# Kernel optimization log

Hardware: AMD Instinct MI355X
Metric: run time of the kernel (lower is better)

## Reference

```python
import jax, jax.numpy as jnp
import numpy as np

N_NODES = 10000
N_EDGES = 80000
F_IN = 128
H1 = 2048
H2 = 2048
H3 = 1024


def _sgconv(x, pos, src, dst, W_in, b_in, W_out, b_out):
    # geo-GCN SpatialGraphConv with hidden_size=1:
    # message(j->i) = relu(Linear(pos_j - pos_i)) * x_j ; aggr='add' ; then Linear out
    rel = pos[src] - pos[dst]                      # [E, 2]  (pos_j - pos_i)
    scale = jax.nn.relu(rel @ W_in + b_in)         # [E, C_in]
    msg = scale * x[src]                           # [E, C_in]
    agg = jax.ops.segment_sum(msg, dst, num_segments=x.shape[0])  # [N, C_in]
    return agg @ W_out + b_out                     # [N, C_out]


def setup_inputs() -> dict:
    key = jax.random.key(0)
    ks = jax.random.split(key, 12)
    x = jax.random.normal(ks[0], (N_NODES, F_IN), dtype=jnp.float32)
    pos = jax.random.normal(ks[1], (N_NODES, 2), dtype=jnp.float32)
    edge_index = jax.random.randint(ks[2], (2, N_EDGES), 0, N_NODES, dtype=jnp.int32)

    def lin(k, fan_in, fan_out):
        lim = 1.0 / np.sqrt(fan_in)
        kw, kb = jax.random.split(k)
        W = jax.random.uniform(kw, (fan_in, fan_out), jnp.float32, -lim, lim)
        b = jax.random.uniform(kb, (fan_out,), jnp.float32, -lim, lim)
        return W, b

    W_in1, b_in1 = lin(ks[3], 2, F_IN)
    W_out1, b_out1 = lin(ks[4], F_IN, H1)
    W_in2, b_in2 = lin(ks[5], 2, H1)
    W_out2, b_out2 = lin(ks[6], H1, H2)
    W_in3, b_in3 = lin(ks[7], 2, H2)
    W_out3, b_out3 = lin(ks[8], H2, H3)

    return {
        "x": x, "pos": pos, "edge_index": edge_index,
        "W_in1": W_in1, "b_in1": b_in1, "W_out1": W_out1, "b_out1": b_out1,
        "W_in2": W_in2, "b_in2": b_in2, "W_out2": W_out2, "b_out2": b_out2,
        "W_in3": W_in3, "b_in3": b_in3, "W_out3": W_out3, "b_out3": b_out3,
    }


def reference(x, pos, edge_index,
              W_in1, b_in1, W_out1, b_out1,
              W_in2, b_in2, W_out2, b_out2,
              W_in3, b_in3, W_out3, b_out3):
    src, dst = edge_index[0], edge_index[1]  # flow source_to_target: j=src, i=dst
    h = jax.nn.relu(_sgconv(x, pos, src, dst, W_in1, b_in1, W_out1, b_out1))
    h = jax.nn.relu(_sgconv(h, pos, src, dst, W_in2, b_in2, W_out2, b_out2))
    h = jax.nn.relu(_sgconv(h, pos, src, dst, W_in3, b_in3, W_out3, b_out3))
    # F.normalize(h, dim=1): L2 normalize rows with eps clamp 1e-12
    norm = jnp.linalg.norm(h, axis=1, keepdims=True)
    return h / jnp.maximum(norm, 1e-12)
```

## Files before the change

### kernel.cpp

```cpp
#include <hip/hip_runtime.h>
#include <hip/hip_bf16.h>

#define DEVI __device__ __forceinline__

constexpr int NN = 10000;
constexpr int NE = 80000;
constexpr int AGG_ROWS = 10240;

typedef __attribute__((ext_vector_type(8))) short bf16x8;
typedef __attribute__((ext_vector_type(4))) float f32x4;

DEVI float blo(unsigned int u) {
  union { unsigned int i; float f; } c; c.i = u << 16; return c.f;
}
DEVI float bhi(unsigned int u) {
  union { unsigned int i; float f; } c; c.i = u & 0xffff0000u; return c.f;
}
DEVI unsigned short f2b(float f) {
  union { float f; unsigned int i; } c; c.f = f;
  unsigned int i = c.i;
  return (unsigned short)((i + 0x7fffu + ((i >> 16) & 1u)) >> 16);
}
DEVI void st1(float* p, float v) { *p = v; }
DEVI void st1(unsigned short* p, float v) { *p = f2b(v); }
DEVI void store8b(unsigned short* p, const float v[8]) {
  int4 pk;
  pk.x = (int)((unsigned)f2b(v[0]) | ((unsigned)f2b(v[1]) << 16));
  pk.y = (int)((unsigned)f2b(v[2]) | ((unsigned)f2b(v[3]) << 16));
  pk.z = (int)((unsigned)f2b(v[4]) | ((unsigned)f2b(v[5]) << 16));
  pk.w = (int)((unsigned)f2b(v[6]) | ((unsigned)f2b(v[7]) << 16));
  *reinterpret_cast<int4*>(p) = pk;
}

DEVI void gload16(const void* g, void* l) {
  __builtin_amdgcn_global_load_lds(
      (const __attribute__((address_space(1))) void*)g,
      (__attribute__((address_space(3))) void*)l, 16, 0, 0);
}

__global__ __launch_bounds__(256)
void hist_kernel(const int* __restrict__ dst, int* __restrict__ cnt) {
  int e = blockIdx.x * 256 + threadIdx.x;
  if (e < NE) atomicAdd(&cnt[dst[e]], 1);
}

__global__ __launch_bounds__(256)
void scan_kernel(const int* __restrict__ cnt, int* __restrict__ off,
                 int* __restrict__ cursor) {
  __shared__ int buf[256];
  __shared__ int carry;
  if (threadIdx.x == 0) carry = 0;
  __syncthreads();
  for (int base = 0; base < NN; base += 256) {
    int i = base + threadIdx.x;
    int v = (i < NN) ? cnt[i] : 0;
    buf[threadIdx.x] = v;
    __syncthreads();
#pragma unroll
    for (int o = 1; o < 256; o <<= 1) {
      int t = (threadIdx.x >= o) ? buf[threadIdx.x - o] : 0;
      __syncthreads();
      buf[threadIdx.x] += t;
      __syncthreads();
    }
    int incl = buf[threadIdx.x];
    int c0 = carry;
    if (i < NN) { int ex = c0 + incl - v; off[i] = ex; cursor[i] = ex; }
    __syncthreads();
    if (threadIdx.x == 255) carry = c0 + incl;
    __syncthreads();
  }
}

__global__ __launch_bounds__(256)
void bucket_kernel(const int* __restrict__ src, const int* __restrict__ dst,
                   const float* __restrict__ pos,
                   int* __restrict__ cursor, float4* __restrict__ epack) {
  int e = blockIdx.x * 256 + threadIdx.x;
  if (e < NE) {
    int s = src[e], d = dst[e];
    int p = atomicAdd(&cursor[d], 1);
    float2 ps = *reinterpret_cast<const float2*>(pos + 2 * s);
    float2 pd = *reinterpret_cast<const float2*>(pos + 2 * d);
    epack[p] = make_float4(ps.x - pd.x, ps.y - pd.y, __int_as_float(s), 0.f);
  }
}

__global__ __launch_bounds__(256)
void transpose_w(const float* __restrict__ W, unsigned short* __restrict__ WT,
                 int K, int N) {
  __shared__ float tile[32][33];
  int tx = threadIdx.x & 31, ty = threadIdx.x >> 5;
  int n0 = blockIdx.x * 32, k0 = blockIdx.y * 32;
#pragma unroll
  for (int j = 0; j < 32; j += 8)
    tile[ty + j][tx] = W[(size_t)(k0 + ty + j) * N + n0 + tx];
  __syncthreads();
#pragma unroll
  for (int j = 0; j < 32; j += 8)
    WT[(size_t)(n0 + ty + j) * K + k0 + tx] = f2b(tile[tx][ty + j]);
}

__global__ __launch_bounds__(256)
void gather_l1(const float* __restrict__ x,
               const int* __restrict__ off, const int* __restrict__ cnt,
               const float4* __restrict__ epack,
               const float* __restrict__ Win, const float* __restrict__ bin,
               unsigned short* __restrict__ agg) {
  constexpr int C = 128;
  int lane = threadIdx.x & 63;
  int i = blockIdx.x * 4 + (threadIdx.x >> 6);
  if (i >= NN) return;
  int c = lane * 2;
  float w00 = Win[c], w01 = Win[c + 1];
  float w10 = Win[C + c], w11 = Win[C + c + 1];
  float b0 = bin[c], b1 = bin[c + 1];
  float a0 = 0.f, a1 = 0.f;
  int s0 = off[i], n = cnt[i];

  float4 e0, e1, e2, e3;
  float2 q0, q1, q2, q3;
  auto ld = [&](int k, float4& e, float2& q) {
    if (k < n) {
      e = epack[s0 + k];
      int s = __float_as_int(e.z);
      q = *reinterpret_cast<const float2*>(x + (size_t)s * C + c);
    }
  };
  auto acc1 = [&](const float4& e, const float2& q) {
    float sc0 = fmaxf(fmaf(e.x, w00, fmaf(e.y, w10, b0)), 0.f);
    float sc1 = fmaxf(fmaf(e.x, w01, fmaf(e.y, w11, b1)), 0.f);
    a0 = fmaf(sc0, q.x, a0);
    a1 = fmaf(sc1, q.y, a1);
  };
  ld(0, e0, q0); ld(1, e1, q1); ld(2, e2, q2); ld(3, e3, q3);
  for (int k = 0; k < n; k += 4) {
    acc1(e0, q0); ld(k + 4, e0, q0);
    if (k + 1 < n) { acc1(e1, q1); } ld(k + 5, e1, q1);
    if (k + 2 < n) { acc1(e2, q2); } ld(k + 6, e2, q2);
    if (k + 3 < n) { acc1(e3, q3); } ld(k + 7, e3, q3);
  }
  unsigned int pk = (unsigned)f2b(a0) | ((unsigned)f2b(a1) << 16);
  *reinterpret_cast<unsigned int*>(agg + (size_t)i * C + c) = pk;
}

__global__ __launch_bounds__(256)
void gather_chunk(const unsigned short* __restrict__ x,
                  const int* __restrict__ off, const int* __restrict__ cnt,
                  const float4* __restrict__ epack,
                  const float* __restrict__ Win, const float* __restrict__ bin,
                  unsigned short* __restrict__ agg, int ngb8) {
  constexpr int C = 2048;
  constexpr int V = 8;
  int wgid = blockIdx.x;
  int half = wgid >= ngb8;
  int base = half ? wgid - ngb8 : wgid;
  int chunk = (base & 7) + (half << 3);
  int grp = base >> 3;
  int lane = threadIdx.x & 63;
  int wid = threadIdx.x >> 6;
  int slot = lane >> 4;
  int l16 = lane & 15;
  int i = grp * 16 + wid * 4 + slot;
  int c = chunk * 128 + l16 * V;

  float w0[V], w1[V], bb[V], acc[V];
#pragma unroll
  for (int j = 0; j < V; ++j) {
    w0[j] = Win[c + j]; w1[j] = Win[C + c + j]; bb[j] = bin[c + j]; acc[j] = 0.f;
  }
  int s0 = off[i], n = cnt[i];

  float4 e0, e1, e2, e3;
  int4 q0, q1, q2, q3;
  auto ld = [&](int k, float4& e, int4& q) {
    if (k < n) {
      e = epack[s0 + k];
      int s = __float_as_int(e.z);
      q = *reinterpret_cast<const int4*>(x + (size_t)s * C + c);
    }
  };
  auto fma8 = [&](const float4& e, const int4& q) {
    float xv[V] = { blo(q.x), bhi(q.x), blo(q.y), bhi(q.y),
                    blo(q.z), bhi(q.z), blo(q.w), bhi(q.w) };
#pragma unroll
    for (int j = 0; j < V; ++j) {
      float sc = fmaxf(fmaf(e.x, w0[j], fmaf(e.y, w1[j], bb[j])), 0.f);
      acc[j] = fmaf(sc, xv[j], acc[j]);
    }
  };
  ld(0, e0, q0); ld(1, e1, q1); ld(2, e2, q2); ld(3, e3, q3);
  for (int k = 0; k < n; k += 4) {
    fma8(e0, q0); ld(k + 4, e0, q0);
    if (k + 1 < n) { fma8(e1, q1); } ld(k + 5, e1, q1);
    if (k + 2 < n) { fma8(e2, q2); } ld(k + 6, e2, q2);
    if (k + 3 < n) { fma8(e3, q3); } ld(k + 7, e3, q3);
  }
  store8b(agg + (size_t)i * C + c, acc);
}

template <typename OT>
__global__ __launch_bounds__(256, 2)
void gemm160(const unsigned short* __restrict__ A,
             const unsigned short* __restrict__ BT,
             const float* __restrict__ bias, OT* __restrict__ out,
             int M, int N, int K) {
  extern __shared__ unsigned short lds[];
  const int t = threadIdx.x;
  const int lane = t & 63, wid = t >> 6;
  const int wr = wid >> 1, wc = wid & 1;

  const int nwg = gridDim.x * gridDim.y;
  const int orig = blockIdx.y * gridDim.x + blockIdx.x;
  const int swz = (orig & 7) * (nwg >> 3) + (orig >> 3);
  const int bx = swz % gridDim.x, by = swz / gridDim.x;
  const int m0 = by * 160, n0 = bx * 128;
  const int nk = K >> 6;

  const int lrow = lane >> 3;
  const int schunk = (lane & 7) ^ lrow;
  const unsigned short* gA = A + (size_t)(m0 + wid * 40 + lrow) * K + schunk * 8;
  const unsigned short* gB = BT + (size_t)(n0 + wid * 32 + lrow) * K + schunk * 8;
  unsigned short* lA = lds + (wid * 5) * 512 + lane * 8;
  unsigned short* lB = lds + 20480 + (wid * 4) * 512 + lane * 8;

  auto STAGE = [&](int buf, int kt) {
    const size_t ko = (size_t)kt << 6;
#pragma unroll
    for (int jj = 0; jj < 5; ++jj)
      gload16(gA + (size_t)(jj * 8) * K + ko, lA + buf * 10240 + jj * 512);
#pragma unroll
    for (int jj = 0; jj < 4; ++jj)
      gload16(gB + (size_t)(jj * 8) * K + ko, lB + buf * 8192 + jj * 512);
  };

  const int frow = lane & 15;
  const int fr7 = frow & 7;
  const int slot0 = ((lane >> 4) ^ fr7) * 8;
  const int slot1 = ((4 + (lane >> 4)) ^ fr7) * 8;
  const int paRow = (wr * 80 + frow) * 64;
  const int pbRow = (wc * 64 + frow) * 64;

  f32x4 acc[5][4];
#pragma unroll
  for (int m = 0; m < 5; ++m)
#pragma unroll
    for (int n = 0; n < 4; ++n) acc[m][n] = 0.f;

  STAGE(0, 0);

  int cur = 0;
  for (int kt = 0; kt < nk; ++kt) {
    if (kt + 1 < nk) {
      STAGE(cur ^ 1, kt + 1);
      asm volatile("s_waitcnt vmcnt(9)" ::: "memory");
    } else {
      asm volatile("s_waitcnt vmcnt(0)" ::: "memory");
    }
    asm volatile("s_barrier" ::: "memory");
    const unsigned short* pa = lds + cur * 10240 + paRow;
    const unsigned short* pb = lds + 20480 + cur * 8192 + pbRow;
#pragma unroll
    for (int ks = 0; ks < 2; ++ks) {
      const int sl = ks ? slot1 : slot0;
      bf16x8 af[5], bf[4];
#pragma unroll
      for (int m = 0; m < 5; ++m)
        af[m] = *reinterpret_cast<const bf16x8*>(pa + m * 1024 + sl);
#pragma unroll
      for (int n = 0; n < 4; ++n)
        bf[n] = *reinterpret_cast<const bf16x8*>(pb + n * 1024 + sl);
      __builtin_amdgcn_s_setprio(1);
#pragma unroll
      for (int m = 0; m < 5; ++m)
#pragma unroll
        for (int n = 0; n < 4; ++n)
          acc[m][n] = __builtin_amdgcn_mfma_f32_16x16x32_bf16(
              af[m], bf[n], acc[m][n], 0, 0, 0);
      __builtin_amdgcn_s_setprio(0);
    }
    asm volatile("s_barrier" ::: "memory");
    cur ^= 1;
  }

  const int ccol = lane & 15;
  const int crow = (lane >> 4) * 4;
  float bv[4];
#pragma unroll
  for (int n = 0; n < 4; ++n)
    bv[n] = bias[n0 + wc * 64 + n * 16 + ccol];
#pragma unroll
  for (int m = 0; m < 5; ++m) {
    int gm0 = m0 + wr * 80 + m * 16 + crow;
#pragma unroll
    for (int r = 0; r < 4; ++r) {
      int gm = gm0 + r;
      if (gm < M) {
        size_t base = (size_t)gm * N + n0 + wc * 64 + ccol;
#pragma unroll
        for (int n = 0; n < 4; ++n)
          st1(out + base + n * 16, fmaxf(acc[m][n][r] + bv[n], 0.f));
      }
    }
  }
}

__global__ __launch_bounds__(256)
void l2norm_kernel(float* __restrict__ out) {
  constexpr int C = 1024;
  float* p = out + (size_t)blockIdx.x * C;
  float4 v = *reinterpret_cast<const float4*>(p + threadIdx.x * 4);
  float s = v.x * v.x + v.y * v.y + v.z * v.z + v.w * v.w;
#pragma unroll
  for (int o = 32; o > 0; o >>= 1) s += __shfl_down(s, o);
  __shared__ float wsum[4];
  if ((threadIdx.x & 63) == 0) wsum[threadIdx.x >> 6] = s;
  __syncthreads();
  float tot = wsum[0] + wsum[1] + wsum[2] + wsum[3];
  float inv = 1.0f / fmaxf(sqrtf(tot), 1e-12f);
  float4 r = make_float4(v.x * inv, v.y * inv, v.z * inv, v.w * inv);
  *reinterpret_cast<float4*>(p + threadIdx.x * 4) = r;
}

extern "C" void kernel_launch(void* const* d_in, const int* in_sizes, int n_in,
                              void* d_out, int out_size, void* d_ws, size_t ws_size,
                              hipStream_t stream) {
  (void)in_sizes; (void)n_in; (void)out_size; (void)ws_size;
  const float* x     = (const float*)d_in[0];
  const float* pos   = (const float*)d_in[1];
  const int*   ei    = (const int*)d_in[2];
  const int*   srcv  = ei;
  const int*   dstv  = ei + NE;
  const float* Win1  = (const float*)d_in[3];
  const float* bin1  = (const float*)d_in[4];
  const float* Wout1 = (const float*)d_in[5];
  const float* bout1 = (const float*)d_in[6];
  const float* Win2  = (const float*)d_in[7];
  const float* bin2  = (const float*)d_in[8];
  const float* Wout2 = (const float*)d_in[9];
  const float* bout2 = (const float*)d_in[10];
  const float* Win3  = (const float*)d_in[11];
  const float* bin3  = (const float*)d_in[12];
  const float* Wout3 = (const float*)d_in[13];
  const float* bout3 = (const float*)d_in[14];
  float* outp = (float*)d_out;

  char* ws = (char*)d_ws;
  unsigned short* aggb = (unsigned short*)ws;
  unsigned short* h1   = (unsigned short*)(ws + 41943040);
  unsigned short* W2T  = (unsigned short*)(ws + 82903040);
  unsigned short* W3T  = (unsigned short*)(ws + 91291648);
  unsigned short* W1T  = (unsigned short*)(ws + 95485952);
  int* cnt    = (int*)(ws + 96010240);
  int* off    = (int*)(ws + 96050240);
  int* cursor = (int*)(ws + 96090240);
  float4* epack = (float4*)(ws + 96130240);
  unsigned short* h2 = (unsigned short*)d_out;

  hipFuncSetAttribute((const void*)gemm160<unsigned short>,
                      hipFuncAttributeMaxDynamicSharedMemorySize, 73728);
  hipFuncSetAttribute((const void*)gemm160<float>,
                      hipFuncAttributeMaxDynamicSharedMemorySize, 73728);

  const dim3 blk(256);
  const int eb = (NE + 255) / 256;
  const int ngb8 = ((NN + 15) / 16) * 8;

  hipMemsetAsync(cnt, 0, NN * sizeof(int), stream);
  hist_kernel<<<eb, blk, 0, stream>>>(dstv, cnt);
  scan_kernel<<<1, blk, 0, stream>>>(cnt, off, cursor);
  bucket_kernel<<<eb, blk, 0, stream>>>(srcv, dstv, pos, cursor, epack);

  transpose_w<<<dim3(2048 / 32, 128 / 32),  blk, 0, stream>>>(Wout1, W1T, 128, 2048);
  transpose_w<<<dim3(2048 / 32, 2048 / 32), blk, 0, stream>>>(Wout2, W2T, 2048, 2048);
  transpose_w<<<dim3(1024 / 32, 2048 / 32), blk, 0, stream>>>(Wout3, W3T, 2048, 1024);

  hipMemsetAsync(aggb + (size_t)NN * 2048, 0, (size_t)(AGG_ROWS - NN) * 2048 * 2, stream);

  gather_l1<<<(NN + 3) / 4, blk, 0, stream>>>(x, off, cnt, epack, Win1, bin1, aggb);
  gemm160<unsigned short><<<dim3(2048 / 128, AGG_ROWS / 160), blk, 73728, stream>>>(
      aggb, W1T, bout1, h1, NN, 2048, 128);

  gather_chunk<<<2 * ngb8, blk, 0, stream>>>(h1, off, cnt, epack, Win2, bin2, aggb, ngb8);
  gemm160<unsigned short><<<dim3(2048 / 128, AGG_ROWS / 160), blk, 73728, stream>>>(
      aggb, W2T, bout2, h2, NN, 2048, 2048);

  gather_chunk<<<2 * ngb8, blk, 0, stream>>>(h2, off, cnt, epack, Win3, bin3, aggb, ngb8);
  gemm160<float><<<dim3(1024 / 128, AGG_ROWS / 160), blk, 73728, stream>>>(
      aggb, W3T, bout3, outp, NN, 1024, 2048);

  l2norm_kernel<<<NN, blk, 0, stream>>>(outp);
}
```

Baseline: 354.1 us.

## Split edge pack into padded SoA arrays and widen GEMM tile to 320 rows

Edge buckets are padded to multiples of four so the gather kernels can load four source indices and relative positions as single vector loads, with padded slots zeroed. This replaces the single-edge software prefetch. The scan becomes a 1024-thread wave-shuffle scan. The GEMM is reworked to 320x128 tiles with a K-step of 32, an unswizzled LDS layout and static shared memory. This doubles per-wave accumulators, which risks register pressure and LDS bank conflicts in exchange for better operand reuse and fewer workgroups.

```diff
diff --git a/kernel.cpp b/kernel.cpp
--- a/kernel.cpp
+++ b/kernel.cpp
@@ -6,6 +6,7 @@
 constexpr int NN = 10000;
 constexpr int NE = 80000;
 constexpr int AGG_ROWS = 10240;
+constexpr int ES_CAP = 110016;
 
 typedef __attribute__((ext_vector_type(8))) short bf16x8;
 typedef __attribute__((ext_vector_type(4))) float f32x4;
@@ -44,30 +45,33 @@
   if (e < NE) atomicAdd(&cnt[dst[e]], 1);
 }
 
-__global__ __launch_bounds__(256)
+__global__ __launch_bounds__(1024)
 void scan_kernel(const int* __restrict__ cnt, int* __restrict__ off,
                  int* __restrict__ cursor) {
-  __shared__ int buf[256];
+  __shared__ int wpart[16];
   __shared__ int carry;
-  if (threadIdx.x == 0) carry = 0;
+  int tid = threadIdx.x, lane = tid & 63, w = tid >> 6;
+  if (tid == 0) carry = 0;
   __syncthreads();
-  for (int base = 0; base < NN; base += 256) {
-    int i = base + threadIdx.x;
-    int v = (i < NN) ? cnt[i] : 0;
-    buf[threadIdx.x] = v;
+  for (int base = 0; base < NN; base += 1024) {
+    int i = base + tid;
+    int v = (i < NN) ? ((cnt[i] + 3) & ~3) : 0;
+    int s = v;
+#pragma unroll
+    for (int o = 1; o < 64; o <<= 1) { int t = __shfl_up(s, o); if (lane >= o) s += t; }
+    if (lane == 63) wpart[w] = s;
     __syncthreads();
-#pragma unroll
-    for (int o = 1; o < 256; o <<= 1) {
-      int t = (threadIdx.x >= o) ? buf[threadIdx.x - o] : 0;
-      __syncthreads();
-      buf[threadIdx.x] += t;
-      __syncthreads();
-    }
-    int incl = buf[threadIdx.x];
-    int c0 = carry;
-    if (i < NN) { int ex = c0 + incl - v; off[i] = ex; cursor[i] = ex; }
+    if (w == 0) {
+      int ws = (lane < 16) ? wpart[lane] : 0;
+#pragma unroll
+      for (int o = 1; o < 16; o <<= 1) { int t = __shfl_up(ws, o); if (lane >= o) ws += t; }
+      if (lane < 16) wpart[lane] = ws;
+    }
     __syncthreads();
-    if (threadIdx.x == 255) carry = c0 + incl;
+    int ex = carry + (w ? wpart[w - 1] : 0) + s - v;
+    if (i < NN) { off[i] = ex; cursor[i] = ex; }
+    __syncthreads();
+    if (tid == 0) carry += wpart[15];
     __syncthreads();
   }
 }
@@ -75,14 +79,16 @@
 __global__ __launch_bounds__(256)
 void bucket_kernel(const int* __restrict__ src, const int* __restrict__ dst,
                    const float* __restrict__ pos,
-                   int* __restrict__ cursor, float4* __restrict__ epack) {
+                   int* __restrict__ cursor, int* __restrict__ es,
+                   float* __restrict__ rel) {
   int e = blockIdx.x * 256 + threadIdx.x;
   if (e < NE) {
     int s = src[e], d = dst[e];
     int p = atomicAdd(&cursor[d], 1);
     float2 ps = *reinterpret_cast<const float2*>(pos + 2 * s);
     float2 pd = *reinterpret_cast<const float2*>(pos + 2 * d);
-    epack[p] = make_float4(ps.x - pd.x, ps.y - pd.y, __int_as_float(s), 0.f);
+    es[p] = s;
+    *reinterpret_cast<float2*>(rel + 2 * p) = make_float2(ps.x - pd.x, ps.y - pd.y);
   }
 }
 
@@ -104,7 +110,7 @@
 __global__ __launch_bounds__(256)
 void gather_l1(const float* __restrict__ x,
                const int* __restrict__ off, const int* __restrict__ cnt,
-               const float4* __restrict__ epack,
+               const int* __restrict__ es, const float* __restrict__ rel,
                const float* __restrict__ Win, const float* __restrict__ bin,
                unsigned short* __restrict__ agg) {
   constexpr int C = 128;
@@ -118,27 +124,34 @@
   float a0 = 0.f, a1 = 0.f;
   int s0 = off[i], n = cnt[i];
 
-  float4 e0, e1, e2, e3;
-  float2 q0, q1, q2, q3;
-  auto ld = [&](int k, float4& e, float2& q) {
-    if (k < n) {
-      e = epack[s0 + k];
-      int s = __float_as_int(e.z);
-      q = *reinterpret_cast<const float2*>(x + (size_t)s * C + c);
-    }
-  };
-  auto acc1 = [&](const float4& e, const float2& q) {
-    float sc0 = fmaxf(fmaf(e.x, w00, fmaf(e.y, w10, b0)), 0.f);
-    float sc1 = fmaxf(fmaf(e.x, w01, fmaf(e.y, w11, b1)), 0.f);
-    a0 = fmaf(sc0, q.x, a0);
-    a1 = fmaf(sc1, q.y, a1);
-  };
-  ld(0, e0, q0); ld(1, e1, q1); ld(2, e2, q2); ld(3, e3, q3);
   for (int k = 0; k < n; k += 4) {
-    acc1(e0, q0); ld(k + 4, e0, q0);
-    if (k + 1 < n) { acc1(e1, q1); } ld(k + 5, e1, q1);
-    if (k + 2 < n) { acc1(e2, q2); } ld(k + 6, e2, q2);
-    if (k + 3 < n) { acc1(e3, q3); } ld(k + 7, e3, q3);
+    int4 s4 = *reinterpret_cast<const int4*>(es + s0 + k);
+    float4 ra = *reinterpret_cast<const float4*>(rel + 2 * (s0 + k));
+    float4 rb = *reinterpret_cast<const float4*>(rel + 2 * (s0 + k) + 4);
+    float2 q0 = *reinterpret_cast<const float2*>(x + (size_t)s4.x * C + c);
+    float2 q1 = *reinterpret_cast<const float2*>(x + (size_t)s4.y * C + c);
+    float2 q2 = *reinterpret_cast<const float2*>(x + (size_t)s4.z * C + c);
+    float2 q3 = *reinterpret_cast<const float2*>(x + (size_t)s4.w * C + c);
+    {
+      float sc0 = fmaxf(fmaf(ra.x, w00, fmaf(ra.y, w10, b0)), 0.f);
+      float sc1 = fmaxf(fmaf(ra.x, w01, fmaf(ra.y, w11, b1)), 0.f);
+      a0 = fmaf(sc0, q0.x, a0); a1 = fmaf(sc1, q0.y, a1);
+    }
+    if (k + 1 < n) {
+      float sc0 = fmaxf(fmaf(ra.z, w00, fmaf(ra.w, w10, b0)), 0.f);
+      float sc1 = fmaxf(fmaf(ra.z, w01, fmaf(ra.w, w11, b1)), 0.f);
+      a0 = fmaf(sc0, q1.x, a0); a1 = fmaf(sc1, q1.y, a1);
+    }
+    if (k + 2 < n) {
+      float sc0 = fmaxf(fmaf(rb.x, w00, fmaf(rb.y, w10, b0)), 0.f);
+      float sc1 = fmaxf(fmaf(rb.x, w01, fmaf(rb.y, w11, b1)), 0.f);
+      a0 = fmaf(sc0, q2.x, a0); a1 = fmaf(sc1, q2.y, a1);
+    }
+    if (k + 3 < n) {
+      float sc0 = fmaxf(fmaf(rb.z, w00, fmaf(rb.w, w10, b0)), 0.f);
+      float sc1 = fmaxf(fmaf(rb.z, w01, fmaf(rb.w, w11, b1)), 0.f);
+      a0 = fmaf(sc0, q3.x, a0); a1 = fmaf(sc1, q3.y, a1);
+    }
   }
   unsigned int pk = (unsigned)f2b(a0) | ((unsigned)f2b(a1) << 16);
   *reinterpret_cast<unsigned int*>(agg + (size_t)i * C + c) = pk;
@@ -147,7 +160,7 @@
 __global__ __launch_bounds__(256)
 void gather_chunk(const unsigned short* __restrict__ x,
                   const int* __restrict__ off, const int* __restrict__ cnt,
-                  const float4* __restrict__ epack,
+                  const int* __restrict__ es, const float* __restrict__ rel,
                   const float* __restrict__ Win, const float* __restrict__ bin,
                   unsigned short* __restrict__ agg, int ngb8) {
   constexpr int C = 2048;
@@ -171,41 +184,38 @@
   }
   int s0 = off[i], n = cnt[i];
 
-  float4 e0, e1, e2, e3;
-  int4 q0, q1, q2, q3;
-  auto ld = [&](int k, float4& e, int4& q) {
-    if (k < n) {
-      e = epack[s0 + k];
-      int s = __float_as_int(e.z);
-      q = *reinterpret_cast<const int4*>(x + (size_t)s * C + c);
-    }
-  };
-  auto fma8 = [&](const float4& e, const int4& q) {
+  auto fma8 = [&](float rx, float ry, const int4& q) {
     float xv[V] = { blo(q.x), bhi(q.x), blo(q.y), bhi(q.y),
                     blo(q.z), bhi(q.z), blo(q.w), bhi(q.w) };
 #pragma unroll
     for (int j = 0; j < V; ++j) {
-      float sc = fmaxf(fmaf(e.x, w0[j], fmaf(e.y, w1[j], bb[j])), 0.f);
+      float sc = fmaxf(fmaf(rx, w0[j], fmaf(ry, w1[j], bb[j])), 0.f);
       acc[j] = fmaf(sc, xv[j], acc[j]);
     }
   };
-  ld(0, e0, q0); ld(1, e1, q1); ld(2, e2, q2); ld(3, e3, q3);
   for (int k = 0; k < n; k += 4) {
-    fma8(e0, q0); ld(k + 4, e0, q0);
-    if (k + 1 < n) { fma8(e1, q1); } ld(k + 5, e1, q1);
-    if (k + 2 < n) { fma8(e2, q2); } ld(k + 6, e2, q2);
-    if (k + 3 < n) { fma8(e3, q3); } ld(k + 7, e3, q3);
+    int4 s4 = *reinterpret_cast<const int4*>(es + s0 + k);
+    float4 ra = *reinterpret_cast<const float4*>(rel + 2 * (s0 + k));
+    float4 rb = *reinterpret_cast<const float4*>(rel + 2 * (s0 + k) + 4);
+    int4 q0 = *reinterpret_cast<const int4*>(x + (size_t)s4.x * C + c);
+    int4 q1 = *reinterpret_cast<const int4*>(x + (size_t)s4.y * C + c);
+    int4 q2 = *reinterpret_cast<const int4*>(x + (size_t)s4.z * C + c);
+    int4 q3 = *reinterpret_cast<const int4*>(x + (size_t)s4.w * C + c);
+    fma8(ra.x, ra.y, q0);
+    if (k + 1 < n) fma8(ra.z, ra.w, q1);
+    if (k + 2 < n) fma8(rb.x, rb.y, q2);
+    if (k + 3 < n) fma8(rb.z, rb.w, q3);
   }
   store8b(agg + (size_t)i * C + c, acc);
 }
 
 template <typename OT>
 __global__ __launch_bounds__(256, 2)
-void gemm160(const unsigned short* __restrict__ A,
+void gemm320(const unsigned short* __restrict__ A,
              const unsigned short* __restrict__ BT,
              const float* __restrict__ bias, OT* __restrict__ out,
              int M, int N, int K) {
-  extern __shared__ unsigned short lds[];
+  __shared__ unsigned short lds[2 * 14336];
   const int t = threadIdx.x;
   const int lane = t & 63, wid = t >> 6;
   const int wr = wid >> 1, wc = wid & 1;
@@ -214,36 +224,34 @@
   const int orig = blockIdx.y * gridDim.x + blockIdx.x;
   const int swz = (orig & 7) * (nwg >> 3) + (orig >> 3);
   const int bx = swz % gridDim.x, by = swz / gridDim.x;
-  const int m0 = by * 160, n0 = bx * 128;
-  const int nk = K >> 6;
-
-  const int lrow = lane >> 3;
-  const int schunk = (lane & 7) ^ lrow;
-  const unsigned short* gA = A + (size_t)(m0 + wid * 40 + lrow) * K + schunk * 8;
-  const unsigned short* gB = BT + (size_t)(n0 + wid * 32 + lrow) * K + schunk * 8;
-  unsigned short* lA = lds + (wid * 5) * 512 + lane * 8;
-  unsigned short* lB = lds + 20480 + (wid * 4) * 512 + lane * 8;
+  const int m0 = by * 320, n0 = bx * 128;
+  const int nk = K >> 5;
+
+  const unsigned short* gA = A + (size_t)(m0 + lane) * K + wid * 8;
+  const unsigned short* gB = BT + (size_t)(n0 + lane) * K + wid * 8;
+  const int lA0 = wid * 2560 + lane * 8;
+  const int lB0 = 10240 + wid * 1024 + lane * 8;
 
   auto STAGE = [&](int buf, int kt) {
-    const size_t ko = (size_t)kt << 6;
+    const unsigned short* ga = gA + kt * 32;
+    const unsigned short* gb = gB + kt * 32;
+    unsigned short* la = lds + buf * 14336 + lA0;
+    unsigned short* lb = lds + buf * 14336 + lB0;
 #pragma unroll
     for (int jj = 0; jj < 5; ++jj)
-      gload16(gA + (size_t)(jj * 8) * K + ko, lA + buf * 10240 + jj * 512);
-#pragma unroll
-    for (int jj = 0; jj < 4; ++jj)
-      gload16(gB + (size_t)(jj * 8) * K + ko, lB + buf * 8192 + jj * 512);
+      gload16(ga + (size_t)(jj * 64) * K, la + jj * 512);
+#pragma unroll
+    for (int jj = 0; jj < 2; ++jj)
+      gload16(gb + (size_t)(jj * 64) * K, lb + jj * 512);
   };
 
-  const int frow = lane & 15;
-  const int fr7 = frow & 7;
-  const int slot0 = ((lane >> 4) ^ fr7) * 8;
-  const int slot1 = ((4 + (lane >> 4)) ^ fr7) * 8;
-  const int paRow = (wr * 80 + frow) * 64;
-  const int pbRow = (wc * 64 + frow) * 64;
-
-  f32x4 acc[5][4];
-#pragma unroll
-  for (int m = 0; m < 5; ++m)
+  const int frow = lane & 15, fch = lane >> 4;
+  const int paOff = fch * 2560 + (wr * 160 + frow) * 8;
+  const int pbOff = 10240 + fch * 1024 + (wc * 64 + frow) * 8;
+
+  f32x4 acc[10][4];
+#pragma unroll
+  for (int m = 0; m < 10; ++m)
 #pragma unroll
     for (int n = 0; n < 4; ++n) acc[m][n] = 0.f;
 
@@ -253,32 +261,27 @@
   for (int kt = 0; kt < nk; ++kt) {
     if (kt + 1 < nk) {
       STAGE(cur ^ 1, kt + 1);
-      asm volatile("s_waitcnt vmcnt(9)" ::: "memory");
+      asm volatile("s_waitcnt vmcnt(7)" ::: "memory");
     } else {
       asm volatile("s_waitcnt vmcnt(0)" ::: "memory");
     }
     asm volatile("s_barrier" ::: "memory");
-    const unsigned short* pa = lds + cur * 10240 + paRow;
-    const unsigned short* pb = lds + 20480 + cur * 8192 + pbRow;
-#pragma unroll
-    for (int ks = 0; ks < 2; ++ks) {
-      const int sl = ks ? slot1 : slot0;
-      bf16x8 af[5], bf[4];
-#pragma unroll
-      for (int m = 0; m < 5; ++m)
-        af[m] = *reinterpret_cast<const bf16x8*>(pa + m * 1024 + sl);
+    const unsigned short* pa = lds + cur * 14336 + paOff;
+    const unsigned short* pb = lds + cur * 14336 + pbOff;
+    bf16x8 bf[4];
+#pragma unroll
+    for (int n = 0; n < 4; ++n)
+      bf[n] = *reinterpret_cast<const bf16x8*>(pb + n * 128);
+    __builtin_amdgcn_s_setprio(1);
+#pragma unroll
+    for (int m = 0; m < 10; ++m) {
+      bf16x8 af = *reinterpret_cast<const bf16x8*>(pa + m * 128);
 #pragma unroll
       for (int n = 0; n < 4; ++n)
-        bf[n] = *reinterpret_cast<const bf16x8*>(pb + n * 1024 + sl);
-      __builtin_amdgcn_s_setprio(1);
-#pragma unroll
-      for (int m = 0; m < 5; ++m)
-#pragma unroll
-        for (int n = 0; n < 4; ++n)
-          acc[m][n] = __builtin_amdgcn_mfma_f32_16x16x32_bf16(
-              af[m], bf[n], acc[m][n], 0, 0, 0);
-      __builtin_amdgcn_s_setprio(0);
-    }
+        acc[m][n] = __builtin_amdgcn_mfma_f32_16x16x32_bf16(
+            af, bf[n], acc[m][n], 0, 0, 0);
+    }
+    __builtin_amdgcn_s_setprio(0);
     asm volatile("s_barrier" ::: "memory");
     cur ^= 1;
   }
@@ -290,8 +293,8 @@
   for (int n = 0; n < 4; ++n)
     bv[n] = bias[n0 + wc * 64 + n * 16 + ccol];
 #pragma unroll
-  for (int m = 0; m < 5; ++m) {
-    int gm0 = m0 + wr * 80 + m * 16 + crow;
+  for (int m = 0; m < 10; ++m) {
+    int gm0 = m0 + wr * 160 + m * 16 + crow;
 #pragma unroll
     for (int r = 0; r < 4; ++r) {
       int gm = gm0 + r;
@@ -354,22 +357,19 @@
   int* cnt    = (int*)(ws + 96010240);
   int* off    = (int*)(ws + 96050240);
   int* cursor = (int*)(ws + 96090240);
-  float4* epack = (float4*)(ws + 96130240);
+  int* es     = (int*)(ws + 96130240);
+  float* rel  = (float*)(ws + 96570304);
   unsigned short* h2 = (unsigned short*)d_out;
-
-  hipFuncSetAttribute((const void*)gemm160<unsigned short>,
-                      hipFuncAttributeMaxDynamicSharedMemorySize, 73728);
-  hipFuncSetAttribute((const void*)gemm160<float>,
-                      hipFuncAttributeMaxDynamicSharedMemorySize, 73728);
 
   const dim3 blk(256);
   const int eb = (NE + 255) / 256;
   const int ngb8 = ((NN + 15) / 16) * 8;
 
   hipMemsetAsync(cnt, 0, NN * sizeof(int), stream);
+  hipMemsetAsync(es, 0, ES_CAP * sizeof(int), stream);
   hist_kernel<<<eb, blk, 0, stream>>>(dstv, cnt);
-  scan_kernel<<<1, blk, 0, stream>>>(cnt, off, cursor);
-  bucket_kernel<<<eb, blk, 0, stream>>>(srcv, dstv, pos, cursor, epack);
+  scan_kernel<<<1, 1024, 0, stream>>>(cnt, off, cursor);
+  bucket_kernel<<<eb, blk, 0, stream>>>(srcv, dstv, pos, cursor, es, rel);
 
   transpose_w<<<dim3(2048 / 32, 128 / 32),  blk, 0, stream>>>(Wout1, W1T, 128, 2048);
   transpose_w<<<dim3(2048 / 32, 2048 / 32), blk, 0, stream>>>(Wout2, W2T, 2048, 2048);
@@ -377,16 +377,16 @@
 
   hipMemsetAsync(aggb + (size_t)NN * 2048, 0, (size_t)(AGG_ROWS - NN) * 2048 * 2, stream);
 
-  gather_l1<<<(NN + 3) / 4, blk, 0, stream>>>(x, off, cnt, epack, Win1, bin1, aggb);
-  gemm160<unsigned short><<<dim3(2048 / 128, AGG_ROWS / 160), blk, 73728, stream>>>(
+  gather_l1<<<(NN + 3) / 4, blk, 0, stream>>>(x, off, cnt, es, rel, Win1, bin1, aggb);
+  gemm320<unsigned short><<<dim3(2048 / 128, AGG_ROWS / 320), blk, 0, stream>>>(
       aggb, W1T, bout1, h1, NN, 2048, 128);
 
-  gather_chunk<<<2 * ngb8, blk, 0, stream>>>(h1, off, cnt, epack, Win2, bin2, aggb, ngb8);
-  gemm160<unsigned short><<<dim3(2048 / 128, AGG_ROWS / 160), blk, 73728, stream>>>(
+  gather_chunk<<<2 * ngb8, blk, 0, stream>>>(h1, off, cnt, es, rel, Win2, bin2, aggb, ngb8);
+  gemm320<unsigned short><<<dim3(2048 / 128, AGG_ROWS / 320), blk, 0, stream>>>(
       aggb, W2T, bout2, h2, NN, 2048, 2048);
 
-  gather_chunk<<<2 * ngb8, blk, 0, stream>>>(h2, off, cnt, epack, Win3, bin3, aggb, ngb8);
-  gemm160<float><<<dim3(1024 / 128, AGG_ROWS / 160), blk, 73728, stream>>>(
+  gather_chunk<<<2 * ngb8, blk, 0, stream>>>(h2, off, cnt, es, rel, Win3, bin3, aggb, ngb8);
+  gemm320<float><<<dim3(1024 / 128, AGG_ROWS / 320), blk, 0, stream>>>(
       aggb, W3T, bout3, outp, NN, 1024, 2048);
 
   l2norm_kernel<<<NN, blk, 0, stream>>>(outp);
```

New measurement: 371.0 us. 4.8% more time.
